# Optimization experiments

Hardware: AMD Instinct MI355X
Metric: run time of the kernel (lower is better)

Reference implementation:

```python
import jax, jax.numpy as jnp
import numpy as np
from jax import lax

L, B, D = 512, 128, 512   # listener frames, batch, listener feature dim
T, E, C, H, V = 200, 384, 128, 512, 46  # decode steps, embed, context, hidden(=E+C), vocab


def setup_inputs() -> dict:
    key = jax.random.key(0)
    ks = jax.random.split(key, 32)
    def p(i, shape, s=0.02):
        return jax.random.normal(ks[i], shape, dtype=jnp.float32) * s
    return {
        "listener_features": jax.random.normal(ks[0], (L, B, D), dtype=jnp.float32),
        "utterance_lengths": jax.random.randint(ks[1], (B,), L // 2, L + 1),
        "transcript": jax.random.randint(ks[2], (T, B), 0, V),
        "embedding": p(3, (V, E), 1.0),
        "w_ih0": p(4, (4 * H, E + C)), "w_hh0": p(5, (4 * H, H)),
        "b_ih0": jnp.zeros((4 * H,), jnp.float32), "b_hh0": jnp.zeros((4 * H,), jnp.float32),
        "w_ih1": p(6, (4 * H, H)), "w_hh1": p(7, (4 * H, H)),
        "b_ih1": jnp.zeros((4 * H,), jnp.float32), "b_hh1": jnp.zeros((4 * H,), jnp.float32),
        "w_ih2": p(8, (4 * H, H)), "w_hh2": p(9, (4 * H, H)),
        "b_ih2": jnp.zeros((4 * H,), jnp.float32), "b_hh2": jnp.zeros((4 * H,), jnp.float32),
        "phi_w": p(10, (C, H)), "phi_b": jnp.zeros((C,), jnp.float32),
        "key_w": p(11, (C, D)), "key_b": jnp.zeros((C,), jnp.float32),
        "value_w": p(12, (C, D)), "value_b": jnp.zeros((C,), jnp.float32),
        "out_w": p(13, (V, H + C)), "out_b": jnp.zeros((V,), jnp.float32),
        "init_hx0": jnp.zeros((1, H), jnp.float32), "init_cx0": jnp.zeros((1, H), jnp.float32),
        "init_hx1": jnp.zeros((1, H), jnp.float32), "init_cx1": jnp.zeros((1, H), jnp.float32),
        "init_hx2": jnp.zeros((1, H), jnp.float32), "init_cx2": jnp.zeros((1, H), jnp.float32),
    }


def _lstm_cell(x, h, c, w_ih, w_hh, b_ih, b_hh):
    gates = x @ w_ih.T + b_ih + h @ w_hh.T + b_hh  # [B,4H]
    i, f, g, o = jnp.split(gates, 4, axis=-1)
    c2 = jax.nn.sigmoid(f) * c + jax.nn.sigmoid(i) * jnp.tanh(g)
    h2 = jax.nn.sigmoid(o) * jnp.tanh(c2)
    return h2, c2


def reference(listener_features, utterance_lengths, transcript, embedding,
              w_ih0, w_hh0, b_ih0, b_hh0, w_ih1, w_hh1, b_ih1, b_hh1,
              w_ih2, w_hh2, b_ih2, b_hh2, phi_w, phi_b, key_w, key_b,
              value_w, value_b, out_w, out_b,
              init_hx0, init_cx0, init_hx1, init_cx1, init_hx2, init_cx2):
    nL, nB = listener_features.shape[0], listener_features.shape[1]
    mask = (jnp.arange(nL)[None, :] < utterance_lengths[:, None]).astype(jnp.float32)  # [B,L]
    # key/value projections are step-invariant (original recomputes them each step; same math)
    keyf = jnp.einsum('lbd,cd->blc', listener_features, key_w) + key_b   # [B,L,C]
    valf = jnp.einsum('lbd,cd->blc', listener_features, value_w) + value_b  # [B,L,C]

    def attend(hx2):
        q = hx2 @ phi_w.T + phi_b                      # [B,C]
        energy = jnp.einsum('bc,blc->bl', q, keyf)     # [B,L]
        a = jax.nn.softmax(energy, axis=-1) * mask
        a = a / jnp.maximum(jnp.sum(a, axis=-1, keepdims=True), 1e-12)  # F.normalize(p=1)
        ctx = jnp.einsum('bl,blc->bc', a, valf)        # [B,C]
        return a, ctx

    hx0 = jnp.broadcast_to(init_hx0, (nB, H)); cx0 = jnp.broadcast_to(init_cx0, (nB, H))
    hx1 = jnp.broadcast_to(init_hx1, (nB, H)); cx1 = jnp.broadcast_to(init_cx1, (nB, H))
    hx2 = jnp.broadcast_to(init_hx2, (nB, H)); cx2 = jnp.broadcast_to(init_cx2, (nB, H))
    _, ctx = attend(hx2)  # initial context from initial decoder state

    # teacher forcing: step t consumes <sos>(=0) then transcript[t-1]
    in_chars = jnp.concatenate([jnp.zeros((1, nB), transcript.dtype), transcript[:-1]], axis=0)  # [T,B]
    emb = embedding[in_chars]  # [T,B,E]

    def step(carry, emb_t):
        hx0, cx0, hx1, cx1, hx2, cx2, ctx = carry
        x = jnp.concatenate([emb_t, ctx], axis=-1)  # [B,E+C]
        hx0, cx0 = _lstm_cell(x, hx0, cx0, w_ih0, w_hh0, b_ih0, b_hh0)
        hx1, cx1 = _lstm_cell(hx0, hx1, cx1, w_ih1, w_hh1, b_ih1, b_hh1)
        hx2, cx2 = _lstm_cell(hx1, hx2, cx2, w_ih2, w_hh2, b_ih2, b_hh2)
        a, ctx = attend(hx2)
        logits = jnp.concatenate([hx2, ctx], axis=-1) @ out_w.T + out_b  # [B,V]
        return (hx0, cx0, hx1, cx1, hx2, cx2, ctx), (logits, a)

    carry0 = (hx0, cx0, hx1, cx1, hx2, cx2, ctx)
    _, (logits, attn) = lax.scan(step, carry0, emb)
    return logits, attn  # [T,B,V], [T,B,L]
```

## Files before the change

kernel.cpp:

```cpp
#include <hip/hip_runtime.h>

typedef unsigned short UST;
typedef unsigned int uint32;
typedef float f32x4 __attribute__((ext_vector_type(4)));
typedef short s16x8 __attribute__((ext_vector_type(8)));


__device__ __forceinline__ float b2f(UST u) {
  uint32 x = ((uint32)u) << 16;
  union { uint32 u; float f; } v; v.u = x; return v.f;
}
__device__ __forceinline__ UST f2bf(float f) {
  union { float f; uint32 u; } v; v.f = f;
  uint32 r = (v.u + 0x7fffu + ((v.u >> 16) & 1u)) >> 16;
  return (UST)r;
}
__device__ __forceinline__ ushort4 f2bf4(float4 v) {
  ushort4 r; r.x = f2bf(v.x); r.y = f2bf(v.y); r.z = f2bf(v.z); r.w = f2bf(v.w); return r;
}
__device__ __forceinline__ float sigf(float x) { return 1.f / (1.f + __expf(-x)); }
__device__ __forceinline__ float tanhf_(float x) { return 2.f / (1.f + __expf(-2.f * x)) - 1.f; }

union U8 { unsigned long long u; ushort4 s; uint2 w; };

__device__ __forceinline__ void st_flag(int* p, int v) {
  __hip_atomic_store(p, v, __ATOMIC_RELAXED, __HIP_MEMORY_SCOPE_AGENT);
}
__device__ __forceinline__ int ld_flag(const int* p) {
  return __hip_atomic_load(p, __ATOMIC_RELAXED, __HIP_MEMORY_SCOPE_AGENT);
}
__device__ __forceinline__ unsigned long long ld8(const void* p) {
  return __hip_atomic_load((const unsigned long long*)p, __ATOMIC_RELAXED, __HIP_MEMORY_SCOPE_AGENT);
}
__device__ __forceinline__ void st4(void* p, uint32 v) {
  __hip_atomic_store((uint32*)p, v, __ATOMIC_RELAXED, __HIP_MEMORY_SCOPE_AGENT);
}
__device__ __forceinline__ uint4 ld16c(const UST* p) {
  U8 a, b; a.u = ld8(p); b.u = ld8(p + 4);
  uint4 v; v.x = a.w.x; v.y = a.w.y; v.z = b.w.x; v.w = b.w.y; return v;
}

__device__ __forceinline__ void signal_flag(int* fl, int idx, int val, int tid) {
  __atomic_signal_fence(__ATOMIC_SEQ_CST);
  __builtin_amdgcn_s_waitcnt(0);
  __atomic_signal_fence(__ATOMIC_SEQ_CST);
  __syncthreads();
  if (tid == 0) st_flag(&fl[idx * 16], val);
}
__device__ __forceinline__ void wait128f(int* fl, int val, int tid, unsigned long long dl) {
  if (tid < 128) {
    while (ld_flag(&fl[tid * 16]) < val) {
      if (__builtin_amdgcn_s_memrealtime() > dl) break;
      __builtin_amdgcn_s_sleep(1);
    }
  }
  __syncthreads();
}
__device__ __forceinline__ void wait64f(int* fl, int val, int tid, unsigned long long dl) {
  if (tid < 64) {
    while (ld_flag(&fl[tid * 16]) < val) {
      if (__builtin_amdgcn_s_memrealtime() > dl) break;
      __builtin_amdgcn_s_sleep(1);
    }
  }
  __syncthreads();
}

struct Args {
  const float* lf; const int* ulen; const int* tr; const float* emb;
  const float* wih0; const float* whh0; const float* bih0; const float* bhh0;
  const float* wih1; const float* whh1; const float* bih1; const float* bhh1;
  const float* wih2; const float* whh2; const float* bih2; const float* bhh2;
  const float* phi_w; const float* phi_b; const float* key_w; const float* key_b;
  const float* val_w; const float* val_b; const float* out_w; const float* out_b;
  const float* ihx0; const float* icx0; const float* ihx1; const float* icx1;
  const float* ihx2; const float* icx2;
  int* bar; UST* wr; UST* xemb; UST* phi_bf; UST* keyfT; UST* valfT;
  UST* hx0; UST* hx1; UST* hx2; UST* ctx; UST* h2h; UST* cxh;
  float* out_logits; float* out_attn;
};

__global__ void __launch_bounds__(256) kprep(Args A) {
  const long N0 = 8192;
  const long N1 = 3L * 2048 * 1024;
  const long N2 = 200L * 128 * 384;
  const long N3 = 128L * 512;
  long total = N0 + N1 + N2 + N3;
  long stride = (long)gridDim.x * blockDim.x;
  for (long ii = (long)blockIdx.x * 256 + threadIdx.x; ii < total; ii += stride) {
    long j = ii;
    if (j < N0) { A.bar[j] = 0; continue; }
    j -= N0;
    if (j < N1) {
      int q = (int)j;
      int i = q & 7, lane = (q >> 3) & 63, nt = (q >> 9) & 1, ks = (q >> 10) & 31;
      int js = (q >> 15) & 63, cell = q >> 21;
      int gr = js * 32 + nt * 16 + (lane & 15);
      int jc = gr >> 2, g = gr & 3, k = ks * 32 + (lane >> 4) * 8 + i;
      const float* wi = cell == 0 ? A.wih0 : cell == 1 ? A.wih1 : A.wih2;
      const float* wh = cell == 0 ? A.whh0 : cell == 1 ? A.whh1 : A.whh2;
      float v;
      if (cell == 0)
        v = (k < 384) ? wi[(g * 512 + jc) * 512 + k]
          : (k < 896) ? wh[(g * 512 + jc) * 512 + k - 384]
                      : wi[(g * 512 + jc) * 512 + k - 512];
      else
        v = (k < 512) ? wi[(g * 512 + jc) * 512 + k] : wh[(g * 512 + jc) * 512 + k - 512];
      A.wr[j] = f2bf(v);
      continue;
    }
    j -= N1;
    if (j < N2) {
      int t = (int)(j / 49152); int r = (int)(j % 49152); int bb = r / 384; int e = r - bb * 384;
      int ch = (t == 0) ? 0 : A.tr[(t - 1) * 128 + bb];
      A.xemb[j] = f2bf(A.emb[ch * 384 + e]);
      continue;
    }
    j -= N2;
    A.phi_bf[j] = f2bf(A.phi_w[j]);
  }
}

__global__ void __launch_bounds__(256) kkv(Args A) {
  __shared__ __attribute__((aligned(16))) char sm[17408 + 34816];
  UST (*A_lds)[136] = (UST(*)[136])sm;
  UST (*W_lds)[136] = (UST(*)[136])(sm + 17408);
  float* sbuf = (float*)(sm + 17408);
  int tid = threadIdx.x, lane = tid & 63, wv = tid >> 6, ln = lane & 15, qd = lane >> 4;
  int blk = blockIdx.x;
  int b = blk >> 4, lt = (blk >> 1) & 7, kv = blk & 1;
  int l0 = lt * 64;
  const float* W = kv ? A.val_w : A.key_w;
  const float* bs = kv ? A.val_b : A.key_b;
  UST* outp = kv ? A.valfT : A.keyfT;
  f32x4 acc[8];
#pragma unroll
  for (int nt = 0; nt < 8; ++nt) {
    float x = bs[nt * 16 + ln];
    f32x4 t; t[0] = x; t[1] = x; t[2] = x; t[3] = x; acc[nt] = t;
  }
  for (int cc = 0; cc < 4; ++cc) {
    int d0 = cc * 128;
#pragma unroll
    for (int it = 0; it < 8; ++it) {
      int idx = it * 256 + tid, row = idx >> 5, seg = idx & 31;
      float4 v = *(const float4*)(A.lf + ((size_t)(l0 + row) * 128 + b) * 512 + d0 + seg * 4);
      *(ushort4*)&A_lds[row][seg * 4] = f2bf4(v);
    }
#pragma unroll
    for (int it = 0; it < 16; ++it) {
      int idx = it * 256 + tid, row = idx >> 5, seg = idx & 31;
      float4 v = *(const float4*)(W + (size_t)row * 512 + d0 + seg * 4);
      *(ushort4*)&W_lds[row][seg * 4] = f2bf4(v);
    }
    __syncthreads();
#pragma unroll
    for (int ks = 0; ks < 4; ++ks) {
      s16x8 av = *(const s16x8*)&A_lds[wv * 16 + ln][ks * 32 + qd * 8];
#pragma unroll
      for (int nt = 0; nt < 8; ++nt) {
        s16x8 bv = *(const s16x8*)&W_lds[nt * 16 + ln][ks * 32 + qd * 8];
        acc[nt] = __builtin_amdgcn_mfma_f32_16x16x32_bf16(av, bv, acc[nt], 0, 0, 0);
      }
    }
    __syncthreads();
  }
#pragma unroll
  for (int nt = 0; nt < 8; ++nt)
#pragma unroll
    for (int r = 0; r < 4; ++r)
      sbuf[(wv * 16 + qd * 4 + r) * 128 + nt * 16 + ln] = acc[nt][r];
  __syncthreads();
  int c2 = tid >> 1, lh = tid & 1;
  for (int g8 = 0; g8 < 4; ++g8) {
    UST tmp[8];
#pragma unroll
    for (int i = 0; i < 8; ++i) tmp[i] = f2bf(sbuf[(lh * 32 + g8 * 8 + i) * 128 + c2]);
    *(uint4*)(outp + ((size_t)b * 128 + c2) * 512 + l0 + lh * 32 + g8 * 8) = *(uint4*)tmp;
  }
}

__device__ __forceinline__ void stage_plain(int cS, int rB, const UST* src, UST (*X)[512]) {
  uint4 rg[16];
#pragma unroll
  for (int it = 0; it < 16; ++it)
    rg[it] = ld16c(src + (it * 4 + rB) * 512 + cS * 8);
  __syncthreads();
#pragma unroll
  for (int it = 0; it < 16; ++it) {
    int r = it * 4 + rB;
    *(uint4*)&X[r][(cS ^ (r & 7)) * 8] = rg[it];
  }
  __syncthreads();
}
template <int SPW>
__device__ __forceinline__ void compute_r(int w, int ln, int qd, int lane,
    const UST* wb, int ksgBase, int chunkBase, UST (*X)[512], f32x4 acc[4][2]) {
#pragma unroll
  for (int j = 0; j < SPW; ++j) {
    int ls = w * SPW + j;
    int ksg = ksgBase + ls;
    s16x8 b0 = *(const s16x8*)(wb + ((size_t)(ksg * 2 + 0) * 64 + lane) * 8);
    s16x8 b1 = *(const s16x8*)(wb + ((size_t)(ksg * 2 + 1) * 64 + lane) * 8);
#pragma unroll
    for (int rt = 0; rt < 4; ++rt) {
      int r = rt * 16 + ln, c = chunkBase + ls * 4 + qd;
      s16x8 av = *(const s16x8*)&X[r][(c ^ (r & 7)) * 8];
      acc[rt][0] = __builtin_amdgcn_mfma_f32_16x16x32_bf16(av, b0, acc[rt][0], 0, 0, 0);
      acc[rt][1] = __builtin_amdgcn_mfma_f32_16x16x32_bf16(av, b1, acc[rt][1], 0, 0, 0);
    }
  }
}
__device__ __forceinline__ void zacc(f32x4 acc[4][2]) {
#pragma unroll
  for (int rt = 0; rt < 4; ++rt)
#pragma unroll
    for (int nt = 0; nt < 2; ++nt) {
      acc[rt][nt][0] = 0.f; acc[rt][nt][1] = 0.f; acc[rt][nt][2] = 0.f; acc[rt][nt][3] = 0.f;
    }
}
__device__ __forceinline__ void cell_epilogue(const Args& A, int cell, int t, int m, int j0,
    int tid, int w, int ln, int qd, f32x4 acc[4][2], float* FB,
    const float* bias8, float* cr, UST* hdst) {
  __syncthreads();
#pragma unroll
  for (int rt = 0; rt < 4; ++rt)
#pragma unroll
    for (int nt = 0; nt < 2; ++nt)
#pragma unroll
      for (int reg = 0; reg < 4; ++reg)
        FB[w * 2112 + (rt * 16 + qd * 4 + reg) * 33 + nt * 16 + ln] = acc[rt][nt][reg];
  __syncthreads();
  int row = tid >> 2, q4 = tid & 3, grow = m * 64 + row;
  uint32 upack = 0;
#pragma unroll
  for (int jj = 0; jj < 2; ++jj) {
    int gc = (q4 * 2 + jj) * 4;
    int o = row * 33 + gc;
    float g0 = FB[o] + FB[2112 + o] + FB[4224 + o] + FB[6336 + o] + bias8[jj * 4 + 0];
    float g1 = FB[o + 1] + FB[2112 + o + 1] + FB[4224 + o + 1] + FB[6336 + o + 1] + bias8[jj * 4 + 1];
    float g2 = FB[o + 2] + FB[2112 + o + 2] + FB[4224 + o + 2] + FB[6336 + o + 2] + bias8[jj * 4 + 2];
    float g3 = FB[o + 3] + FB[2112 + o + 3] + FB[4224 + o + 3] + FB[6336 + o + 3] + bias8[jj * 4 + 3];
    float cn = sigf(g1) * cr[jj] + sigf(g0) * tanhf_(g2);
    float hv = sigf(g3) * tanhf_(cn);
    cr[jj] = cn;
    upack |= ((uint32)f2bf(hv)) << (16 * jj);
  }
  st4(hdst + grow * 512 + j0 + q4 * 2, upack);
  if (cell == 2) *(uint32*)(A.h2h + ((size_t)t * 128 + grow) * 512 + j0 + q4 * 2) = upack;
}

__device__ __forceinline__ void attend_f(const Args& A, int t, int p, int b, int tid,
    int lane, int wv, char* smraw, const uint4 (&rgK)[32], const uint4 (&rgV)[32]) {
  float* att_h = (float*)smraw;
  float* att_q = att_h + 512;
  float* att_c = att_q + 256;
  float* att_red = att_c + 128;
  float (*e_part)[512] = (float(*)[512])(att_red + 16);
  const UST* hx2p = A.hx2 + p * 65536;
  if (tid < 128) {
    U8 v; v.u = ld8(hx2p + b * 512 + tid * 4);
    att_h[tid * 4 + 0] = b2f(v.s.x); att_h[tid * 4 + 1] = b2f(v.s.y);
    att_h[tid * 4 + 2] = b2f(v.s.z); att_h[tid * 4 + 3] = b2f(v.s.w);
  }
  __syncthreads();
  int c = tid & 127, half = tid >> 7;
  {
    float acc = half ? 0.f : A.phi_b[c];
    const UST* pr = A.phi_bf + c * 512 + half * 256;
    const float* hh = att_h + half * 256;
#pragma unroll 4
    for (int k = 0; k < 256; k += 8) {
      uint4 v = *(const uint4*)(pr + k);
      const UST* us = (const UST*)&v;
#pragma unroll
      for (int i = 0; i < 8; ++i) acc += b2f(us[i]) * hh[k + i];
    }
    att_q[tid] = acc;
  }
  __syncthreads();
  if (tid < 128) att_q[tid] += att_q[tid + 128];
  __syncthreads();
  {
    int cg = tid >> 6, lg = tid & 63;
    float ep[8] = {0, 0, 0, 0, 0, 0, 0, 0};
#pragma unroll
    for (int i = 0; i < 32; ++i) {
      float qv = att_q[cg * 32 + i];
      const UST* us = (const UST*)&rgK[i];
#pragma unroll
      for (int j = 0; j < 8; ++j) ep[j] += qv * b2f(us[j]);
    }
#pragma unroll
    for (int i = 0; i < 8; ++i) e_part[cg][lg * 8 + i] = ep[i];
  }
  __syncthreads();
  float e0 = e_part[0][2 * tid] + e_part[1][2 * tid] + e_part[2][2 * tid] + e_part[3][2 * tid];
  float e1 = e_part[0][2 * tid + 1] + e_part[1][2 * tid + 1] + e_part[2][2 * tid + 1] + e_part[3][2 * tid + 1];
  float mx = fmaxf(e0, e1);
#pragma unroll
  for (int off = 32; off; off >>= 1) mx = fmaxf(mx, __shfl_xor(mx, off));
  if (lane == 0) att_red[wv] = mx;
  __syncthreads();
  mx = fmaxf(fmaxf(att_red[0], att_red[1]), fmaxf(att_red[2], att_red[3]));
  int len = A.ulen[b];
  float x0 = (2 * tid < len) ? __expf(e0 - mx) : 0.f;
  float x1 = (2 * tid + 1 < len) ? __expf(e1 - mx) : 0.f;
  float s = x0 + x1;
#pragma unroll
  for (int off = 32; off; off >>= 1) s += __shfl_xor(s, off);
  if (lane == 0) att_red[8 + wv] = s;
  __syncthreads();
  s = att_red[8] + att_red[9] + att_red[10] + att_red[11];
  float inv = 1.f / fmaxf(s, 1e-12f);
  float a0 = x0 * inv, a1 = x1 * inv;
  float* esm = &e_part[0][0];
  esm[2 * tid] = a0; esm[2 * tid + 1] = a1;
  if (t >= 0) {
    float2 st; st.x = a0; st.y = a1;
    *(float2*)(A.out_attn + ((size_t)t * 128 + b) * 512 + 2 * tid) = st;
  }
  __syncthreads();
  {
    float acc = 0.f;
    const float* aa = esm + half * 256;
#pragma unroll
    for (int i = 0; i < 32; ++i) {
      const UST* us = (const UST*)&rgV[i];
#pragma unroll
      for (int j = 0; j < 8; ++j) acc += aa[i * 8 + j] * b2f(us[j]);
    }
    att_q[tid] = acc;
  }
  __syncthreads();
  if (tid < 128) att_c[tid] = att_q[tid] + att_q[tid + 128];
  __syncthreads();
  if (tid < 64) {
    float cv0 = att_c[2 * tid], cv1 = att_c[2 * tid + 1];
    uint32 u = (uint32)f2bf(cv0) | ((uint32)f2bf(cv1) << 16);
    st4(A.ctx + p * 16384 + b * 128 + 2 * tid, u);
    if (t >= 0) *(uint32*)(A.cxh + ((size_t)t * 128 + b) * 128 + 2 * tid) = u;
  }
}

__global__ void __launch_bounds__(256) kmain(Args A) {
  __shared__ __attribute__((aligned(16))) char smraw[65536];
  unsigned long long dl = __builtin_amdgcn_s_memrealtime() + 100000000ull;
  int blk = blockIdx.x, tid = threadIdx.x;
  int lane = tid & 63, w = tid >> 6, ln = lane & 15, qd = lane >> 4;
  int* c0f = A.bar;
  int* c1f = A.bar + 2048;
  int* c2f = A.bar + 4096;
  int* attf = A.bar + 6144;
  if (blk < 128) {
    UST (*X)[512] = (UST(*)[512])smraw;
    float* FB = (float*)smraw;
    int js = ((blk >> 4) << 3) | (blk & 7);
    int m = (blk >> 3) & 1;
    int j0 = js * 8;
    int sid = m * 64 + js;
    int* mc0 = c0f + m * 1024;
    int* mc1 = c1f + m * 1024;
    int* mc2 = c2f + m * 1024;
    int* mat = attf + m * 1024;
    int cS = tid & 63, rB = tid >> 6;
    float bias[3][8]; float cr[3][2];
    {
      const float* bihA[3] = {A.bih0, A.bih1, A.bih2};
      const float* bhhA[3] = {A.bhh0, A.bhh1, A.bhh2};
      const float* icxA[3] = {A.icx0, A.icx1, A.icx2};
      const float* ihxA[3] = {A.ihx0, A.ihx1, A.ihx2};
      UST* hxA[3] = {A.hx0, A.hx1, A.hx2};
      int q4 = tid & 3;
#pragma unroll
      for (int cI = 0; cI < 3; ++cI) {
#pragma unroll
        for (int jj = 0; jj < 2; ++jj) {
          int col = j0 + q4 * 2 + jj;
          for (int g = 0; g < 4; ++g)
            bias[cI][jj * 4 + g] = bihA[cI][g * 512 + col] + bhhA[cI][g * 512 + col];
          cr[cI][jj] = icxA[cI][col];
        }
        int row = tid >> 2, grow = m * 64 + row, col0 = j0 + q4 * 2;
        uint32 u = (uint32)f2bf(ihxA[cI][col0]) | ((uint32)f2bf(ihxA[cI][col0 + 1]) << 16);
        st4(hxA[cI] + 65536 + grow * 512 + col0, u);
      }
    }
    signal_flag(c2f, sid, 1, tid);
    wait128f(c2f, 1, tid, dl);
    const UST* wrj0 = A.wr + (size_t)js * 32768;
    const UST* wrj1 = wrj0 + 2097152;
    const UST* wrj2 = wrj0 + 4194304;
    f32x4 acc0[4][2], acc1[4][2], acc2[4][2];
    for (int t = 0; t < 200; ++t) {
      int p = t & 1, po = p ^ 1;
      const UST* xe = A.xemb + (size_t)t * 49152 + m * 64 * 384;
      const UST* h0r = A.hx0 + po * 65536 + m * 64 * 512;
      const UST* h1r = A.hx1 + po * 65536 + m * 64 * 512;
      const UST* h2r = A.hx2 + po * 65536 + m * 64 * 512;
      const UST* cxr = A.ctx + po * 16384 + m * 64 * 128;
      zacc(acc0); zacc(acc1); zacc(acc2);
      {
        uint4 rg[16];
        if (cS < 48) {
#pragma unroll
          for (int it = 0; it < 16; ++it)
            rg[it] = *(const uint4*)(xe + (it * 4 + rB) * 384 + cS * 8);
        } else {
#pragma unroll
          for (int it = 0; it < 16; ++it)
            rg[it] = ld16c(h0r + (it * 4 + rB) * 512 + (cS - 48) * 8);
        }
        __syncthreads();
#pragma unroll
        for (int it = 0; it < 16; ++it) {
          int r = it * 4 + rB;
          *(uint4*)&X[r][(cS ^ (r & 7)) * 8] = rg[it];
        }
        __syncthreads();
      }
      compute_r<4>(w, ln, qd, lane, wrj0, 0, 0, X, acc0);
      {
        uint4 rg[16];
        if (cS < 48) {
#pragma unroll
          for (int it = 0; it < 16; ++it)
            rg[it] = ld16c(h0r + (it * 4 + rB) * 512 + (cS + 16) * 8);
        }
        __syncthreads();
        if (cS < 48) {
#pragma unroll
          for (int it = 0; it < 16; ++it) {
            int r = it * 4 + rB;
            *(uint4*)&X[r][(cS ^ (r & 7)) * 8] = rg[it];
          }
        }
        __syncthreads();
      }
      compute_r<3>(w, ln, qd, lane, wrj0, 16, 0, X, acc0);
      stage_plain(cS, rB, h1r, X);
      compute_r<4>(w, ln, qd, lane, wrj1, 16, 0, X, acc1);
      wait64f(mc2, t + 1, tid, dl);
      stage_plain(cS, rB, h2r, X);
      compute_r<4>(w, ln, qd, lane, wrj2, 16, 0, X, acc2);
      wait64f(mat, t + 1, tid, dl);
      {
        uint4 rg[16];
        if (cS >= 48) {
#pragma unroll
          for (int it = 0; it < 16; ++it)
            rg[it] = ld16c(cxr + (it * 4 + rB) * 128 + (cS - 48) * 8);
#pragma unroll
          for (int it = 0; it < 16; ++it) {
            int r = it * 4 + rB;
            *(uint4*)&X[r][(cS ^ (r & 7)) * 8] = rg[it];
          }
        }
        __syncthreads();
      }
      compute_r<1>(w, ln, qd, lane, wrj0, 28, 48, X, acc0);
      cell_epilogue(A, 0, t, m, j0, tid, w, ln, qd, acc0, FB, bias[0], cr[0], A.hx0 + p * 65536);
      signal_flag(c0f, sid, t + 2, tid);
      const UST* h0n = A.hx0 + p * 65536 + m * 64 * 512;
      wait64f(mc0, t + 2, tid, dl);
      stage_plain(cS, rB, h0n, X);
      compute_r<4>(w, ln, qd, lane, wrj1, 0, 0, X, acc1);
      cell_epilogue(A, 1, t, m, j0, tid, w, ln, qd, acc1, FB, bias[1], cr[1], A.hx1 + p * 65536);
      signal_flag(c1f, sid, t + 2, tid);
      const UST* h1n = A.hx1 + p * 65536 + m * 64 * 512;
      wait64f(mc1, t + 2, tid, dl);
      stage_plain(cS, rB, h1n, X);
      compute_r<4>(w, ln, qd, lane, wrj2, 0, 0, X, acc2);
      cell_epilogue(A, 2, t, m, j0, tid, w, ln, qd, acc2, FB, bias[2], cr[2], A.hx2 + p * 65536);
      signal_flag(c2f, sid, t + 2, tid);
    }
  } else {
    int b = blk - 128;
    int* mc2a = c2f + (b >> 6) * 1024;
    uint4 rgK[32], rgV[32];
    {
      int cg = tid >> 6, lg = tid & 63;
      const UST* kb = A.keyfT + (size_t)b * 65536 + lg * 8;
#pragma unroll
      for (int i = 0; i < 32; ++i)
        rgK[i] = *(const uint4*)(kb + (size_t)(cg * 32 + i) * 512);
      int c = tid & 127, half = tid >> 7;
      const UST* vb = A.valfT + (size_t)b * 65536 + (size_t)c * 512 + half * 256;
#pragma unroll
      for (int i = 0; i < 32; ++i)
        rgV[i] = *(const uint4*)(vb + i * 8);
    }
    wait128f(c2f, 1, tid, dl);
    attend_f(A, -1, 1, b, tid, lane, w, smraw, rgK, rgV);
    signal_flag(attf, b, 1, tid);
    for (int t = 0; t < 200; ++t) {
      wait64f(mc2a, t + 2, tid, dl);
      attend_f(A, t, t & 1, b, tid, lane, w, smraw, rgK, rgV);
      signal_flag(attf, b, t + 2, tid);
    }
  }
}

__global__ void __launch_bounds__(256) kepi(Args A) {
  __shared__ UST ow[46 * 648];
  __shared__ float ob[46];
  int t = blockIdx.x, tid = threadIdx.x;
  for (int i = tid; i < 46 * 640; i += 256) {
    int v = i / 640, k = i - v * 640; ow[v * 648 + k] = f2bf(A.out_w[i]);
  }
  if (tid < 46) ob[tid] = A.out_b[tid];
  __syncthreads();
  for (int oi = tid; oi < 128 * 46; oi += 256) {
    int bb = oi / 46, v = oi - bb * 46;
    const UST* xh = A.h2h + ((size_t)t * 128 + bb) * 512;
    const UST* xc = A.cxh + ((size_t)t * 128 + bb) * 128;
    const UST* wrow = &ow[v * 648];
    float acc = ob[v];
    for (int k = 0; k < 512; k += 8) {
      uint4 xv = *(const uint4*)(xh + k);
      uint4 wv4 = *(const uint4*)(wrow + k);
      const UST* xs = (const UST*)&xv; const UST* wl = (const UST*)&wv4;
#pragma unroll
      for (int i = 0; i < 8; ++i) acc += b2f(xs[i]) * b2f(wl[i]);
    }
    for (int k = 0; k < 128; k += 8) {
      uint4 xv = *(const uint4*)(xc + k);
      uint4 wv4 = *(const uint4*)(wrow + 512 + k);
      const UST* xs = (const UST*)&xv; const UST* wl = (const UST*)&wv4;
#pragma unroll
      for (int i = 0; i < 8; ++i) acc += b2f(xs[i]) * b2f(wl[i]);
    }
    A.out_logits[((size_t)t * 128 + bb) * 46 + v] = acc;
  }
}

extern "C" void kernel_launch(void* const* d_in, const int* in_sizes, int n_in,
                              void* d_out, int out_size, void* d_ws, size_t ws_size,
                              hipStream_t stream) {
  (void)in_sizes; (void)n_in; (void)out_size; (void)ws_size;
  Args a;
  a.lf = (const float*)d_in[0]; a.ulen = (const int*)d_in[1]; a.tr = (const int*)d_in[2];
  a.emb = (const float*)d_in[3];
  a.wih0 = (const float*)d_in[4]; a.whh0 = (const float*)d_in[5]; a.bih0 = (const float*)d_in[6]; a.bhh0 = (const float*)d_in[7];
  a.wih1 = (const float*)d_in[8]; a.whh1 = (const float*)d_in[9]; a.bih1 = (const float*)d_in[10]; a.bhh1 = (const float*)d_in[11];
  a.wih2 = (const float*)d_in[12]; a.whh2 = (const float*)d_in[13]; a.bih2 = (const float*)d_in[14]; a.bhh2 = (const float*)d_in[15];
  a.phi_w = (const float*)d_in[16]; a.phi_b = (const float*)d_in[17];
  a.key_w = (const float*)d_in[18]; a.key_b = (const float*)d_in[19];
  a.val_w = (const float*)d_in[20]; a.val_b = (const float*)d_in[21];
  a.out_w = (const float*)d_in[22]; a.out_b = (const float*)d_in[23];
  a.ihx0 = (const float*)d_in[24]; a.icx0 = (const float*)d_in[25];
  a.ihx1 = (const float*)d_in[26]; a.icx1 = (const float*)d_in[27];
  a.ihx2 = (const float*)d_in[28]; a.icx2 = (const float*)d_in[29];
  char* ws = (char*)d_ws;
  a.bar    = (int*)ws;
  a.wr     = (UST*)(ws + 32768);
  a.xemb   = (UST*)(ws + 12615680);
  a.phi_bf = (UST*)(ws + 32276480);
  a.keyfT  = (UST*)(ws + 32407552);
  a.valfT  = (UST*)(ws + 49184768);
  a.hx0    = (UST*)(ws + 65961984);
  a.hx1    = (UST*)(ws + 66224128);
  a.hx2    = (UST*)(ws + 66486272);
  a.ctx    = (UST*)(ws + 66748416);
  a.h2h    = (UST*)(ws + 66813952);
  a.cxh    = (UST*)(ws + 93028352);
  a.out_logits = (float*)d_out;
  a.out_attn   = (float*)d_out + 1177600;
  kprep<<<4096, 256, 0, stream>>>(a);
  kkv<<<2048, 256, 0, stream>>>(a);
  kmain<<<256, 256, 0, stream>>>(a);
  kepi<<<200, 256, 0, stream>>>(a);
}
```

Before: 7.196 ms.

## Reuse staged hidden states to precompute next-step recurrent partial sums

```diff
diff --git a/kernel.cpp b/kernel.cpp
--- a/kernel.cpp
+++ b/kernel.cpp
@@ -193,6 +193,34 @@
   }
   __syncthreads();
 }
+__device__ __forceinline__ void stage_emb(int cS, int rB, const UST* xe, UST (*X)[512]) {
+  if (cS < 48) {
+    uint4 rg[16];
+#pragma unroll
+    for (int it = 0; it < 16; ++it)
+      rg[it] = *(const uint4*)(xe + (it * 4 + rB) * 384 + cS * 8);
+#pragma unroll
+    for (int it = 0; it < 16; ++it) {
+      int r = it * 4 + rB;
+      *(uint4*)&X[r][(cS ^ (r & 7)) * 8] = rg[it];
+    }
+  }
+  __syncthreads();
+}
+__device__ __forceinline__ void stage_ctx(int cS, int rB, const UST* cxr, UST (*X)[512]) {
+  if (cS >= 48) {
+    uint4 rg[16];
+#pragma unroll
+    for (int it = 0; it < 16; ++it)
+      rg[it] = ld16c(cxr + (it * 4 + rB) * 128 + (cS - 48) * 8);
+#pragma unroll
+    for (int it = 0; it < 16; ++it) {
+      int r = it * 4 + rB;
+      *(uint4*)&X[r][(cS ^ (r & 7)) * 8] = rg[it];
+    }
+  }
+  __syncthreads();
+}
 template <int SPW>
 __device__ __forceinline__ void compute_r(int w, int ln, int qd, int lane,
     const UST* wb, int ksgBase, int chunkBase, UST (*X)[512], f32x4 acc[4][2]) {
@@ -218,6 +246,12 @@
     for (int nt = 0; nt < 2; ++nt) {
       acc[rt][nt][0] = 0.f; acc[rt][nt][1] = 0.f; acc[rt][nt][2] = 0.f; acc[rt][nt][3] = 0.f;
     }
+}
+__device__ __forceinline__ void cacc(f32x4 dst[4][2], const f32x4 src[4][2]) {
+#pragma unroll
+  for (int rt = 0; rt < 4; ++rt)
+#pragma unroll
+    for (int nt = 0; nt < 2; ++nt) dst[rt][nt] = src[rt][nt];
 }
 __device__ __forceinline__ void cell_epilogue(const Args& A, int cell, int t, int m, int j0,
     int tid, int w, int ln, int qd, f32x4 acc[4][2], float* FB,
@@ -343,7 +377,7 @@
   }
 }
 
-__global__ void __launch_bounds__(256) kmain(Args A) {
+__global__ void __launch_bounds__(256, 1) kmain(Args A) {
   __shared__ __attribute__((aligned(16))) char smraw[65536];
   unsigned long long dl = __builtin_amdgcn_s_memrealtime() + 100000000ull;
   int blk = blockIdx.x, tid = threadIdx.x;
@@ -391,88 +425,52 @@
     const UST* wrj0 = A.wr + (size_t)js * 32768;
     const UST* wrj1 = wrj0 + 2097152;
     const UST* wrj2 = wrj0 + 4194304;
-    f32x4 acc0[4][2], acc1[4][2], acc2[4][2];
+    f32x4 acc0[4][2], acc1[4][2], acc2[4][2], acc0n[4][2], acc1n[4][2];
+    zacc(acc0); zacc(acc1); zacc(acc2); zacc(acc0n); zacc(acc1n);
+    {
+      const UST* xe0 = A.xemb + m * 64 * 384;
+      const UST* h0i = A.hx0 + 65536 + m * 64 * 512;
+      const UST* h1i = A.hx1 + 65536 + m * 64 * 512;
+      stage_emb(cS, rB, xe0, X);
+      compute_r<3>(w, ln, qd, lane, wrj0, 0, 0, X, acc0);
+      stage_plain(cS, rB, h0i, X);
+      compute_r<4>(w, ln, qd, lane, wrj0, 12, 0, X, acc0);
+      stage_plain(cS, rB, h1i, X);
+      compute_r<4>(w, ln, qd, lane, wrj1, 16, 0, X, acc1);
+    }
     for (int t = 0; t < 200; ++t) {
       int p = t & 1, po = p ^ 1;
-      const UST* xe = A.xemb + (size_t)t * 49152 + m * 64 * 384;
-      const UST* h0r = A.hx0 + po * 65536 + m * 64 * 512;
-      const UST* h1r = A.hx1 + po * 65536 + m * 64 * 512;
       const UST* h2r = A.hx2 + po * 65536 + m * 64 * 512;
       const UST* cxr = A.ctx + po * 16384 + m * 64 * 128;
-      zacc(acc0); zacc(acc1); zacc(acc2);
-      {
-        uint4 rg[16];
-        if (cS < 48) {
-#pragma unroll
-          for (int it = 0; it < 16; ++it)
-            rg[it] = *(const uint4*)(xe + (it * 4 + rB) * 384 + cS * 8);
-        } else {
-#pragma unroll
-          for (int it = 0; it < 16; ++it)
-            rg[it] = ld16c(h0r + (it * 4 + rB) * 512 + (cS - 48) * 8);
-        }
-        __syncthreads();
-#pragma unroll
-        for (int it = 0; it < 16; ++it) {
-          int r = it * 4 + rB;
-          *(uint4*)&X[r][(cS ^ (r & 7)) * 8] = rg[it];
-        }
-        __syncthreads();
-      }
-      compute_r<4>(w, ln, qd, lane, wrj0, 0, 0, X, acc0);
-      {
-        uint4 rg[16];
-        if (cS < 48) {
-#pragma unroll
-          for (int it = 0; it < 16; ++it)
-            rg[it] = ld16c(h0r + (it * 4 + rB) * 512 + (cS + 16) * 8);
-        }
-        __syncthreads();
-        if (cS < 48) {
-#pragma unroll
-          for (int it = 0; it < 16; ++it) {
-            int r = it * 4 + rB;
-            *(uint4*)&X[r][(cS ^ (r & 7)) * 8] = rg[it];
-          }
-        }
-        __syncthreads();
-      }
-      compute_r<3>(w, ln, qd, lane, wrj0, 16, 0, X, acc0);
-      stage_plain(cS, rB, h1r, X);
-      compute_r<4>(w, ln, qd, lane, wrj1, 16, 0, X, acc1);
       wait64f(mc2, t + 1, tid, dl);
       stage_plain(cS, rB, h2r, X);
       compute_r<4>(w, ln, qd, lane, wrj2, 16, 0, X, acc2);
       wait64f(mat, t + 1, tid, dl);
-      {
-        uint4 rg[16];
-        if (cS >= 48) {
-#pragma unroll
-          for (int it = 0; it < 16; ++it)
-            rg[it] = ld16c(cxr + (it * 4 + rB) * 128 + (cS - 48) * 8);
-#pragma unroll
-          for (int it = 0; it < 16; ++it) {
-            int r = it * 4 + rB;
-            *(uint4*)&X[r][(cS ^ (r & 7)) * 8] = rg[it];
-          }
-        }
-        __syncthreads();
-      }
+      stage_ctx(cS, rB, cxr, X);
       compute_r<1>(w, ln, qd, lane, wrj0, 28, 48, X, acc0);
       cell_epilogue(A, 0, t, m, j0, tid, w, ln, qd, acc0, FB, bias[0], cr[0], A.hx0 + p * 65536);
       signal_flag(c0f, sid, t + 2, tid);
+      if (t < 199) {
+        const UST* xe1 = A.xemb + (size_t)(t + 1) * 49152 + m * 64 * 384;
+        stage_emb(cS, rB, xe1, X);
+        compute_r<3>(w, ln, qd, lane, wrj0, 0, 0, X, acc0n);
+      }
       const UST* h0n = A.hx0 + p * 65536 + m * 64 * 512;
       wait64f(mc0, t + 2, tid, dl);
       stage_plain(cS, rB, h0n, X);
       compute_r<4>(w, ln, qd, lane, wrj1, 0, 0, X, acc1);
+      compute_r<4>(w, ln, qd, lane, wrj0, 12, 0, X, acc0n);
       cell_epilogue(A, 1, t, m, j0, tid, w, ln, qd, acc1, FB, bias[1], cr[1], A.hx1 + p * 65536);
       signal_flag(c1f, sid, t + 2, tid);
       const UST* h1n = A.hx1 + p * 65536 + m * 64 * 512;
       wait64f(mc1, t + 2, tid, dl);
       stage_plain(cS, rB, h1n, X);
       compute_r<4>(w, ln, qd, lane, wrj2, 0, 0, X, acc2);
+      compute_r<4>(w, ln, qd, lane, wrj1, 16, 0, X, acc1n);
       cell_epilogue(A, 2, t, m, j0, tid, w, ln, qd, acc2, FB, bias[2], cr[2], A.hx2 + p * 65536);
       signal_flag(c2f, sid, t + 2, tid);
+      cacc(acc0, acc0n); cacc(acc1, acc1n);
+      zacc(acc0n); zacc(acc1n); zacc(acc2);
     }
   } else {
     int b = blk - 128;
```

After: 8.743 ms. +21.5%, slower.

## Replace block-wide flag barriers with per-wave fine-grained dependency polling

Applied to the files above, without the earlier changes.

```diff
diff --git a/kernel.cpp b/kernel.cpp
--- a/kernel.cpp
+++ b/kernel.cpp
@@ -49,15 +49,6 @@
 }
 __device__ __forceinline__ void wait128f(int* fl, int val, int tid, unsigned long long dl) {
   if (tid < 128) {
-    while (ld_flag(&fl[tid * 16]) < val) {
-      if (__builtin_amdgcn_s_memrealtime() > dl) break;
-      __builtin_amdgcn_s_sleep(1);
-    }
-  }
-  __syncthreads();
-}
-__device__ __forceinline__ void wait64f(int* fl, int val, int tid, unsigned long long dl) {
-  if (tid < 64) {
     while (ld_flag(&fl[tid * 16]) < val) {
       if (__builtin_amdgcn_s_memrealtime() > dl) break;
       __builtin_amdgcn_s_sleep(1);
@@ -193,6 +184,87 @@
   }
   __syncthreads();
 }
+__device__ __forceinline__ void stage_wv(int w, int lane, int* fl, int val,
+    const UST* src, UST (*X)[512], unsigned long long dl) {
+  int cW = w * 16 + (lane & 15), rW = lane >> 4;
+  while (ld_flag(&fl[cW * 16]) < val) {
+    if (__builtin_amdgcn_s_memrealtime() > dl) break;
+    __builtin_amdgcn_s_sleep(1);
+  }
+  uint4 rg[16];
+#pragma unroll
+  for (int it = 0; it < 16; ++it)
+    rg[it] = ld16c(src + (it * 4 + rW) * 512 + cW * 8);
+#pragma unroll
+  for (int it = 0; it < 16; ++it) {
+    int r = it * 4 + rW;
+    *(uint4*)&X[r][(cW ^ (r & 7)) * 8] = rg[it];
+  }
+}
+__device__ __forceinline__ void stage_embh0(int cS, int rB, const UST* xe, const UST* h0r,
+                                            UST (*X)[512]) {
+  uint4 rg[16];
+  if (cS < 48) {
+#pragma unroll
+    for (int it = 0; it < 16; ++it)
+      rg[it] = *(const uint4*)(xe + (it * 4 + rB) * 384 + cS * 8);
+  } else {
+#pragma unroll
+    for (int it = 0; it < 16; ++it)
+      rg[it] = ld16c(h0r + (it * 4 + rB) * 512 + (cS - 48) * 8);
+  }
+  __syncthreads();
+#pragma unroll
+  for (int it = 0; it < 16; ++it) {
+    int r = it * 4 + rB;
+    *(uint4*)&X[r][(cS ^ (r & 7)) * 8] = rg[it];
+  }
+  __syncthreads();
+}
+__device__ __forceinline__ void stage_h0b(int cS, int rB, const UST* h0r, UST (*X)[512]) {
+  uint4 rg[16];
+  if (cS < 48) {
+#pragma unroll
+    for (int it = 0; it < 16; ++it)
+      rg[it] = ld16c(h0r + (it * 4 + rB) * 512 + (cS + 16) * 8);
+  }
+  __syncthreads();
+  if (cS < 48) {
+#pragma unroll
+    for (int it = 0; it < 16; ++it) {
+      int r = it * 4 + rB;
+      *(uint4*)&X[r][(cS ^ (r & 7)) * 8] = rg[it];
+    }
+  }
+  __syncthreads();
+}
+__device__ __forceinline__ void stage_ctx_poll(int cS, int rB, int* fl, int val,
+    const UST* cxr, UST (*X)[512], unsigned long long dl) {
+  uint4 rg[16];
+  if (cS >= 48) {
+    for (;;) {
+      bool ok = true;
+#pragma unroll
+      for (int it = 0; it < 16; ++it)
+        ok &= (ld_flag(&fl[(it * 4 + rB) * 16]) >= val);
+      if (ok) break;
+      if (__builtin_amdgcn_s_memrealtime() > dl) break;
+      __builtin_amdgcn_s_sleep(1);
+    }
+#pragma unroll
+    for (int it = 0; it < 16; ++it)
+      rg[it] = ld16c(cxr + (it * 4 + rB) * 128 + (cS - 48) * 8);
+  }
+  __syncthreads();
+  if (cS >= 48) {
+#pragma unroll
+    for (int it = 0; it < 16; ++it) {
+      int r = it * 4 + rB;
+      *(uint4*)&X[r][(cS ^ (r & 7)) * 8] = rg[it];
+    }
+  }
+  __syncthreads();
+}
 template <int SPW>
 __device__ __forceinline__ void compute_r(int w, int ln, int qd, int lane,
     const UST* wb, int ksgBase, int chunkBase, UST (*X)[512], f32x4 acc[4][2]) {
@@ -251,7 +323,8 @@
 }
 
 __device__ __forceinline__ void attend_f(const Args& A, int t, int p, int b, int tid,
-    int lane, int wv, char* smraw, const uint4 (&rgK)[32], const uint4 (&rgV)[32]) {
+    int lane, int wv, char* smraw, const uint4 (&rgK)[32], const uint4 (&rgV)[32],
+    int* pf, int pv, unsigned long long dl) {
   float* att_h = (float*)smraw;
   float* att_q = att_h + 512;
   float* att_c = att_q + 256;
@@ -259,6 +332,11 @@
   float (*e_part)[512] = (float(*)[512])(att_red + 16);
   const UST* hx2p = A.hx2 + p * 65536;
   if (tid < 128) {
+    const int* fp = &pf[(tid >> 1) * 16];
+    while (ld_flag(fp) < pv) {
+      if (__builtin_amdgcn_s_memrealtime() > dl) break;
+      __builtin_amdgcn_s_sleep(1);
+    }
     U8 v; v.u = ld8(hx2p + b * 512 + tid * 4);
     att_h[tid * 4 + 0] = b2f(v.s.x); att_h[tid * 4 + 1] = b2f(v.s.y);
     att_h[tid * 4 + 2] = b2f(v.s.z); att_h[tid * 4 + 3] = b2f(v.s.w);
@@ -400,76 +478,25 @@
       const UST* h2r = A.hx2 + po * 65536 + m * 64 * 512;
       const UST* cxr = A.ctx + po * 16384 + m * 64 * 128;
       zacc(acc0); zacc(acc1); zacc(acc2);
-      {
-        uint4 rg[16];
-        if (cS < 48) {
-#pragma unroll
-          for (int it = 0; it < 16; ++it)
-            rg[it] = *(const uint4*)(xe + (it * 4 + rB) * 384 + cS * 8);
-        } else {
-#pragma unroll
-          for (int it = 0; it < 16; ++it)
-            rg[it] = ld16c(h0r + (it * 4 + rB) * 512 + (cS - 48) * 8);
-        }
-        __syncthreads();
-#pragma unroll
-        for (int it = 0; it < 16; ++it) {
-          int r = it * 4 + rB;
-          *(uint4*)&X[r][(cS ^ (r & 7)) * 8] = rg[it];
-        }
-        __syncthreads();
-      }
+      stage_embh0(cS, rB, xe, h0r, X);
       compute_r<4>(w, ln, qd, lane, wrj0, 0, 0, X, acc0);
-      {
-        uint4 rg[16];
-        if (cS < 48) {
-#pragma unroll
-          for (int it = 0; it < 16; ++it)
-            rg[it] = ld16c(h0r + (it * 4 + rB) * 512 + (cS + 16) * 8);
-        }
-        __syncthreads();
-        if (cS < 48) {
-#pragma unroll
-          for (int it = 0; it < 16; ++it) {
-            int r = it * 4 + rB;
-            *(uint4*)&X[r][(cS ^ (r & 7)) * 8] = rg[it];
-          }
-        }
-        __syncthreads();
-      }
+      stage_h0b(cS, rB, h0r, X);
       compute_r<3>(w, ln, qd, lane, wrj0, 16, 0, X, acc0);
       stage_plain(cS, rB, h1r, X);
       compute_r<4>(w, ln, qd, lane, wrj1, 16, 0, X, acc1);
-      wait64f(mc2, t + 1, tid, dl);
-      stage_plain(cS, rB, h2r, X);
+      stage_wv(w, lane, mc2, t + 1, h2r, X, dl);
       compute_r<4>(w, ln, qd, lane, wrj2, 16, 0, X, acc2);
-      wait64f(mat, t + 1, tid, dl);
-      {
-        uint4 rg[16];
-        if (cS >= 48) {
-#pragma unroll
-          for (int it = 0; it < 16; ++it)
-            rg[it] = ld16c(cxr + (it * 4 + rB) * 128 + (cS - 48) * 8);
-#pragma unroll
-          for (int it = 0; it < 16; ++it) {
-            int r = it * 4 + rB;
-            *(uint4*)&X[r][(cS ^ (r & 7)) * 8] = rg[it];
-          }
-        }
-        __syncthreads();
-      }
+      stage_ctx_poll(cS, rB, mat, t + 1, cxr, X, dl);
       compute_r<1>(w, ln, qd, lane, wrj0, 28, 48, X, acc0);
       cell_epilogue(A, 0, t, m, j0, tid, w, ln, qd, acc0, FB, bias[0], cr[0], A.hx0 + p * 65536);
       signal_flag(c0f, sid, t + 2, tid);
       const UST* h0n = A.hx0 + p * 65536 + m * 64 * 512;
-      wait64f(mc0, t + 2, tid, dl);
-      stage_plain(cS, rB, h0n, X);
+      stage_wv(w, lane, mc0, t + 2, h0n, X, dl);
       compute_r<4>(w, ln, qd, lane, wrj1, 0, 0, X, acc1);
       cell_epilogue(A, 1, t, m, j0, tid, w, ln, qd, acc1, FB, bias[1], cr[1], A.hx1 + p * 65536);
       signal_flag(c1f, sid, t + 2, tid);
       const UST* h1n = A.hx1 + p * 65536 + m * 64 * 512;
-      wait64f(mc1, t + 2, tid, dl);
-      stage_plain(cS, rB, h1n, X);
+      stage_wv(w, lane, mc1, t + 2, h1n, X, dl);
       compute_r<4>(w, ln, qd, lane, wrj2, 0, 0, X, acc2);
       cell_epilogue(A, 2, t, m, j0, tid, w, ln, qd, acc2, FB, bias[2], cr[2], A.hx2 + p * 65536);
       signal_flag(c2f, sid, t + 2, tid);
@@ -490,12 +517,10 @@
       for (int i = 0; i < 32; ++i)
         rgV[i] = *(const uint4*)(vb + i * 8);
     }
-    wait128f(c2f, 1, tid, dl);
-    attend_f(A, -1, 1, b, tid, lane, w, smraw, rgK, rgV);
+    attend_f(A, -1, 1, b, tid, lane, w, smraw, rgK, rgV, mc2a, 1, dl);
     signal_flag(attf, b, 1, tid);
     for (int t = 0; t < 200; ++t) {
-      wait64f(mc2a, t + 2, tid, dl);
-      attend_f(A, t, t & 1, b, tid, lane, w, smraw, rgK, rgV);
+      attend_f(A, t, t & 1, b, tid, lane, w, smraw, rgK, rgV, mc2a, t + 2, dl);
       signal_flag(attf, b, t + 2, tid);
     }
   }
```

Measured after the change: 6.709 ms. 6.8% less time.

## Load MFMA A-operands directly from global and poll only needed producer flags

Applied to the files above, without the earlier changes.

```diff
diff --git a/kernel.cpp b/kernel.cpp
--- a/kernel.cpp
+++ b/kernel.cpp
@@ -22,6 +22,7 @@
 __device__ __forceinline__ float tanhf_(float x) { return 2.f / (1.f + __expf(-2.f * x)) - 1.f; }
 
 union U8 { unsigned long long u; ushort4 s; uint2 w; };
+union UU16 { uint4 u; s16x8 v; };
 
 __device__ __forceinline__ void st_flag(int* p, int v) {
   __hip_atomic_store(p, v, __ATOMIC_RELAXED, __HIP_MEMORY_SCOPE_AGENT);
@@ -56,14 +57,30 @@
   }
   __syncthreads();
 }
-__device__ __forceinline__ void wait64f(int* fl, int val, int tid, unsigned long long dl) {
-  if (tid < 64) {
-    while (ld_flag(&fl[tid * 16]) < val) {
-      if (__builtin_amdgcn_s_memrealtime() > dl) break;
-      __builtin_amdgcn_s_sleep(1);
-    }
-  }
-  __syncthreads();
+template <int SPW>
+__device__ __forceinline__ void poll_cols(int w, int qd, int* fl, int val,
+                                          unsigned long long dl) {
+  int base = (w * SPW) * 4 + qd;
+  for (;;) {
+    bool ok = true;
+#pragma unroll
+    for (int j = 0; j < SPW; ++j)
+      ok &= (ld_flag(&fl[(base + j * 4) * 16]) >= val);
+    if (ok) break;
+    if (__builtin_amdgcn_s_memrealtime() > dl) break;
+    __builtin_amdgcn_s_sleep(1);
+  }
+}
+__device__ __forceinline__ void poll_rows(int ln, int* fl, int val, unsigned long long dl) {
+  for (;;) {
+    bool ok = true;
+#pragma unroll
+    for (int rt = 0; rt < 4; ++rt)
+      ok &= (ld_flag(&fl[(rt * 16 + ln) * 16]) >= val);
+    if (ok) break;
+    if (__builtin_amdgcn_s_memrealtime() > dl) break;
+    __builtin_amdgcn_s_sleep(1);
+  }
 }
 
 struct Args {
@@ -180,34 +197,31 @@
   }
 }
 
-__device__ __forceinline__ void stage_plain(int cS, int rB, const UST* src, UST (*X)[512]) {
-  uint4 rg[16];
-#pragma unroll
-  for (int it = 0; it < 16; ++it)
-    rg[it] = ld16c(src + (it * 4 + rB) * 512 + cS * 8);
-  __syncthreads();
-#pragma unroll
-  for (int it = 0; it < 16; ++it) {
-    int r = it * 4 + rB;
-    *(uint4*)&X[r][(cS ^ (r & 7)) * 8] = rg[it];
-  }
-  __syncthreads();
-}
 template <int SPW>
-__device__ __forceinline__ void compute_r(int w, int ln, int qd, int lane,
-    const UST* wb, int ksgBase, int chunkBase, UST (*X)[512], f32x4 acc[4][2]) {
+__device__ __forceinline__ void load_c(int w, int ln, int qd, const UST* src, int rowStride,
+                                       int colOff, s16x8 af[4][4]) {
 #pragma unroll
   for (int j = 0; j < SPW; ++j) {
-    int ls = w * SPW + j;
-    int ksg = ksgBase + ls;
+    int c = (w * SPW + j) * 4 + qd + colOff;
+#pragma unroll
+    for (int rt = 0; rt < 4; ++rt) {
+      UU16 u; u.u = ld16c(src + (rt * 16 + ln) * rowStride + c * 8);
+      af[j][rt] = u.v;
+    }
+  }
+}
+template <int SPW>
+__device__ __forceinline__ void compute_d(int w, int ln, int qd, int lane,
+    const UST* wb, int ksgBase, const s16x8 af[4][4], f32x4 acc[4][2]) {
+#pragma unroll
+  for (int j = 0; j < SPW; ++j) {
+    int ksg = ksgBase + w * SPW + j;
     s16x8 b0 = *(const s16x8*)(wb + ((size_t)(ksg * 2 + 0) * 64 + lane) * 8);
     s16x8 b1 = *(const s16x8*)(wb + ((size_t)(ksg * 2 + 1) * 64 + lane) * 8);
 #pragma unroll
     for (int rt = 0; rt < 4; ++rt) {
-      int r = rt * 16 + ln, c = chunkBase + ls * 4 + qd;
-      s16x8 av = *(const s16x8*)&X[r][(c ^ (r & 7)) * 8];
-      acc[rt][0] = __builtin_amdgcn_mfma_f32_16x16x32_bf16(av, b0, acc[rt][0], 0, 0, 0);
-      acc[rt][1] = __builtin_amdgcn_mfma_f32_16x16x32_bf16(av, b1, acc[rt][1], 0, 0, 0);
+      acc[rt][0] = __builtin_amdgcn_mfma_f32_16x16x32_bf16(af[j][rt], b0, acc[rt][0], 0, 0, 0);
+      acc[rt][1] = __builtin_amdgcn_mfma_f32_16x16x32_bf16(af[j][rt], b1, acc[rt][1], 0, 0, 0);
     }
   }
 }
@@ -251,7 +265,8 @@
 }
 
 __device__ __forceinline__ void attend_f(const Args& A, int t, int p, int b, int tid,
-    int lane, int wv, char* smraw, const uint4 (&rgK)[32], const uint4 (&rgV)[32]) {
+    int lane, int wv, char* smraw, const uint4 (&rgK)[32], const uint4 (&rgV)[32],
+    int* pf, int pv, unsigned long long dl) {
   float* att_h = (float*)smraw;
   float* att_q = att_h + 512;
   float* att_c = att_q + 256;
@@ -259,6 +274,11 @@
   float (*e_part)[512] = (float(*)[512])(att_red + 16);
   const UST* hx2p = A.hx2 + p * 65536;
   if (tid < 128) {
+    const int* fp = &pf[(tid >> 1) * 16];
+    while (ld_flag(fp) < pv) {
+      if (__builtin_amdgcn_s_memrealtime() > dl) break;
+      __builtin_amdgcn_s_sleep(1);
+    }
     U8 v; v.u = ld8(hx2p + b * 512 + tid * 4);
     att_h[tid * 4 + 0] = b2f(v.s.x); att_h[tid * 4 + 1] = b2f(v.s.y);
     att_h[tid * 4 + 2] = b2f(v.s.z); att_h[tid * 4 + 3] = b2f(v.s.w);
@@ -343,7 +363,7 @@
   }
 }
 
-__global__ void __launch_bounds__(256) kmain(Args A) {
+__global__ void __launch_bounds__(256, 1) kmain(Args A) {
   __shared__ __attribute__((aligned(16))) char smraw[65536];
   unsigned long long dl = __builtin_amdgcn_s_memrealtime() + 100000000ull;
   int blk = blockIdx.x, tid = threadIdx.x;
@@ -353,7 +373,6 @@
   int* c2f = A.bar + 4096;
   int* attf = A.bar + 6144;
   if (blk < 128) {
-    UST (*X)[512] = (UST(*)[512])smraw;
     float* FB = (float*)smraw;
     int js = ((blk >> 4) << 3) | (blk & 7);
     int m = (blk >> 3) & 1;
@@ -363,7 +382,6 @@
     int* mc1 = c1f + m * 1024;
     int* mc2 = c2f + m * 1024;
     int* mat = attf + m * 1024;
-    int cS = tid & 63, rB = tid >> 6;
     float bias[3][8]; float cr[3][2];
     {
       const float* bihA[3] = {A.bih0, A.bih1, A.bih2};
@@ -392,6 +410,7 @@
     const UST* wrj1 = wrj0 + 2097152;
     const UST* wrj2 = wrj0 + 4194304;
     f32x4 acc0[4][2], acc1[4][2], acc2[4][2];
+    s16x8 af[4][4];
     for (int t = 0; t < 200; ++t) {
       int p = t & 1, po = p ^ 1;
       const UST* xe = A.xemb + (size_t)t * 49152 + m * 64 * 384;
@@ -400,77 +419,49 @@
       const UST* h2r = A.hx2 + po * 65536 + m * 64 * 512;
       const UST* cxr = A.ctx + po * 16384 + m * 64 * 128;
       zacc(acc0); zacc(acc1); zacc(acc2);
-      {
-        uint4 rg[16];
-        if (cS < 48) {
-#pragma unroll
-          for (int it = 0; it < 16; ++it)
-            rg[it] = *(const uint4*)(xe + (it * 4 + rB) * 384 + cS * 8);
-        } else {
-#pragma unroll
-          for (int it = 0; it < 16; ++it)
-            rg[it] = ld16c(h0r + (it * 4 + rB) * 512 + (cS - 48) * 8);
-        }
-        __syncthreads();
-#pragma unroll
-        for (int it = 0; it < 16; ++it) {
-          int r = it * 4 + rB;
-          *(uint4*)&X[r][(cS ^ (r & 7)) * 8] = rg[it];
-        }
-        __syncthreads();
-      }
-      compute_r<4>(w, ln, qd, lane, wrj0, 0, 0, X, acc0);
-      {
-        uint4 rg[16];
-        if (cS < 48) {
-#pragma unroll
-          for (int it = 0; it < 16; ++it)
-            rg[it] = ld16c(h0r + (it * 4 + rB) * 512 + (cS + 16) * 8);
-        }
-        __syncthreads();
-        if (cS < 48) {
-#pragma unroll
-          for (int it = 0; it < 16; ++it) {
-            int r = it * 4 + rB;
-            *(uint4*)&X[r][(cS ^ (r & 7)) * 8] = rg[it];
+      if (w < 3) {
+#pragma unroll
+        for (int j = 0; j < 4; ++j) {
+          int cc = (w * 4 + j) * 4 + qd;
+#pragma unroll
+          for (int rt = 0; rt < 4; ++rt) {
+            UU16 u; u.u = *(const uint4*)(xe + (rt * 16 + ln) * 384 + cc * 8);
+            af[j][rt] = u.v;
           }
         }
-        __syncthreads();
+      } else {
+        load_c<4>(w, ln, qd, h0r, 512, -48, af);
       }
-      compute_r<3>(w, ln, qd, lane, wrj0, 16, 0, X, acc0);
-      stage_plain(cS, rB, h1r, X);
-      compute_r<4>(w, ln, qd, lane, wrj1, 16, 0, X, acc1);
-      wait64f(mc2, t + 1, tid, dl);
-      stage_plain(cS, rB, h2r, X);
-      compute_r<4>(w, ln, qd, lane, wrj2, 16, 0, X, acc2);
-      wait64f(mat, t + 1, tid, dl);
+      compute_d<4>(w, ln, qd, lane, wrj0, 0, af, acc0);
+      load_c<3>(w, ln, qd, h0r, 512, 16, af);
+      compute_d<3>(w, ln, qd, lane, wrj0, 16, af, acc0);
+      load_c<4>(w, ln, qd, h1r, 512, 0, af);
+      compute_d<4>(w, ln, qd, lane, wrj1, 16, af, acc1);
+      poll_cols<4>(w, qd, mc2, t + 1, dl);
+      load_c<4>(w, ln, qd, h2r, 512, 0, af);
+      compute_d<4>(w, ln, qd, lane, wrj2, 16, af, acc2);
+      poll_rows(ln, mat, t + 1, dl);
       {
-        uint4 rg[16];
-        if (cS >= 48) {
-#pragma unroll
-          for (int it = 0; it < 16; ++it)
-            rg[it] = ld16c(cxr + (it * 4 + rB) * 128 + (cS - 48) * 8);
-#pragma unroll
-          for (int it = 0; it < 16; ++it) {
-            int r = it * 4 + rB;
-            *(uint4*)&X[r][(cS ^ (r & 7)) * 8] = rg[it];
-          }
+        int cc = w * 4 + qd;
+#pragma unroll
+        for (int rt = 0; rt < 4; ++rt) {
+          UU16 u; u.u = ld16c(cxr + (rt * 16 + ln) * 128 + cc * 8);
+          af[0][rt] = u.v;
         }
-        __syncthreads();
       }
-      compute_r<1>(w, ln, qd, lane, wrj0, 28, 48, X, acc0);
+      compute_d<1>(w, ln, qd, lane, wrj0, 28, af, acc0);
       cell_epilogue(A, 0, t, m, j0, tid, w, ln, qd, acc0, FB, bias[0], cr[0], A.hx0 + p * 65536);
       signal_flag(c0f, sid, t + 2, tid);
       const UST* h0n = A.hx0 + p * 65536 + m * 64 * 512;
-      wait64f(mc0, t + 2, tid, dl);
-      stage_plain(cS, rB, h0n, X);
-      compute_r<4>(w, ln, qd, lane, wrj1, 0, 0, X, acc1);
+      poll_cols<4>(w, qd, mc0, t + 2, dl);
+      load_c<4>(w, ln, qd, h0n, 512, 0, af);
+      compute_d<4>(w, ln, qd, lane, wrj1, 0, af, acc1);
       cell_epilogue(A, 1, t, m, j0, tid, w, ln, qd, acc1, FB, bias[1], cr[1], A.hx1 + p * 65536);
       signal_flag(c1f, sid, t + 2, tid);
       const UST* h1n = A.hx1 + p * 65536 + m * 64 * 512;
-      wait64f(mc1, t + 2, tid, dl);
-      stage_plain(cS, rB, h1n, X);
-      compute_r<4>(w, ln, qd, lane, wrj2, 0, 0, X, acc2);
+      poll_cols<4>(w, qd, mc1, t + 2, dl);
+      load_c<4>(w, ln, qd, h1n, 512, 0, af);
+      compute_d<4>(w, ln, qd, lane, wrj2, 0, af, acc2);
       cell_epilogue(A, 2, t, m, j0, tid, w, ln, qd, acc2, FB, bias[2], cr[2], A.hx2 + p * 65536);
       signal_flag(c2f, sid, t + 2, tid);
     }
@@ -490,12 +481,10 @@
       for (int i = 0; i < 32; ++i)
         rgV[i] = *(const uint4*)(vb + i * 8);
     }
-    wait128f(c2f, 1, tid, dl);
-    attend_f(A, -1, 1, b, tid, lane, w, smraw, rgK, rgV);
+    attend_f(A, -1, 1, b, tid, lane, w, smraw, rgK, rgV, mc2a, 1, dl);
     signal_flag(attf, b, 1, tid);
     for (int t = 0; t < 200; ++t) {
-      wait64f(mc2a, t + 2, tid, dl);
-      attend_f(A, t, t & 1, b, tid, lane, w, smraw, rgK, rgV);
+      attend_f(A, t, t & 1, b, tid, lane, w, smraw, rgK, rgV, mc2a, t + 2, dl);
       signal_flag(attf, b, t + 2, tid);
     }
   }
```

Measured after the change: 7.558 ms. +5.0%, slower.
